# Kernel optimization log

Hardware: AMD Instinct MI355X
Metric: run time of the kernel (lower is better)

Reference implementation:

```python
import jax, jax.numpy as jnp
import numpy as np

BN_EPS = 1e-5

def setup_inputs() -> dict:
    key = jax.random.key(0)
    ks = jax.random.split(key, 4)
    N, C, T, V, H = 32, 64, 512, 25, 3
    x = jax.random.normal(ks[0], (N, C, T, V), dtype=jnp.float32)
    A = jax.random.normal(ks[1], (H, V, V), dtype=jnp.float32)
    # per-head 1x1 conv weights (conv_branch_init-like small std) and biases
    W = jax.random.normal(ks[2], (H, C, C), dtype=jnp.float32) * 0.05
    b = jax.random.normal(ks[3], (H, C), dtype=jnp.float32) * 0.05
    gamma = jnp.ones((C,), dtype=jnp.float32)
    beta = jnp.zeros((C,), dtype=jnp.float32)
    return {"x": x, "A": A, "W": W, "b": b, "gamma": gamma, "beta": beta}

def reference(x, A, W, b, gamma, beta):
    # x: [N,C,T,V], A: [H,V,V], W: [H,Cout,Cin], b: [H,Cout]
    # per-head graph conv: z_h[n,c,t,v] = sum_u A[h,v,u] * x[n,c,t,u]
    z = jnp.einsum('hvu,nctu->hnctv', A, x)
    # per-head 1x1 conv (channel mix) then sum over heads; biases sum too
    out = jnp.einsum('hoc,hnctv->notv', W, z) + b.sum(axis=0)[None, :, None, None]
    # BatchNorm2d (training-mode batch stats, biased variance) over (N,T,V)
    mean = out.mean(axis=(0, 2, 3), keepdims=True)
    var = out.var(axis=(0, 2, 3), keepdims=True)
    out = gamma[None, :, None, None] * (out - mean) * jax.lax.rsqrt(var + BN_EPS) \
          + beta[None, :, None, None]
    # residual (in_channels == out_channels -> identity down) + ReLU
    return jnp.maximum(out + x, 0.0)
```

## Files before the change

kernel.cpp:

```cpp
#include <hip/hip_runtime.h>
#include <hip/hip_bf16.h>

#define N_DIM 32
#define C_DIM 64
#define T_DIM 512
#define V_DIM 25
#define H_DIM 3
#define TT 8
#define GPB 4
#define NBLK1 512
#define NTGRP 2048
#define NTV (N_DIM * T_DIM * V_DIM)
#define NTOT (N_DIM * C_DIM * T_DIM * V_DIM)
#define XPITCH 76
#define XROWS 208
#define TILE_SH 1792
#define SITER 13
#define BN_EPS 1e-5f

typedef float f32x4 __attribute__((ext_vector_type(4)));
typedef short bf16x8 __attribute__((ext_vector_type(8)));
typedef short s16x4 __attribute__((ext_vector_type(4)));

__device__ __forceinline__ short f2bf(float f) {
    __hip_bfloat16 h = __float2bfloat16(f);
    return __builtin_bit_cast(short, h);
}
__device__ __forceinline__ float bf2f(short s) {
    return __uint_as_float(((unsigned)(unsigned short)s) << 16);
}

__device__ __forceinline__ bf16x8 ld_bf8(const short* p) {
    s16x4 a = *(const s16x4*)p;
    s16x4 b = *(const s16x4*)(p + 4);
    bf16x8 r;
    r[0] = a[0]; r[1] = a[1]; r[2] = a[2]; r[3] = a[3];
    r[4] = b[0]; r[5] = b[1]; r[6] = b[2]; r[7] = b[3];
    return r;
}

__global__ __launch_bounds__(256) void gcn_pack(
    const float* __restrict__ A, const float* __restrict__ W,
    short* __restrict__ wpack, short* __restrict__ apack)
{
    const int b   = blockIdx.x;
    const int tid = threadIdx.x;
    const int l15 = tid & 15, hi = (tid >> 4) & 3, w = tid >> 6;
    if (b < 6) {
        int h = b >> 1, s = b & 1;
        const float* wp = W + h * 4096 + (16 * w + l15) * 64 + s * 32 + hi * 8;
        bf16x8 f;
        #pragma unroll
        for (int i = 0; i < 8; ++i) f[i] = f2bf(wp[i]);
        *(bf16x8*)(wpack + ((size_t)b * 256 + tid) * 8) = f;
    } else {
        int bb = b - 6, h = bb >> 1, vt = bb & 1;
        int v = vt * 16 + l15;
        bf16x8 f;
        #pragma unroll
        for (int i = 0; i < 8; ++i) {
            int u = hi * 8 + i;
            f[i] = (v < 25 && u < 25) ? f2bf(A[h * 625 + v * 25 + u]) : (short)0;
        }
        *(bf16x8*)(apack + ((size_t)bb * 256 + tid) * 8) = f;
    }
}

__device__ __forceinline__ void stage_load(float (&fr)[SITER][4],
                                           const float* __restrict__ xg, int tid)
{
    #pragma unroll
    for (int k = 0; k < SITER; ++k) {
        int e = tid + k * 256;
        if (k < SITER - 1 || e < 3200) {
            int cg = e / 200, tu = e - cg * 200;
            const float* p = xg + cg * 51200 + tu;
            fr[k][0] = p[0];
            fr[k][1] = p[12800];
            fr[k][2] = p[25600];
            fr[k][3] = p[38400];
        }
    }
}
__device__ __forceinline__ void stage_write(const float (&fr)[SITER][4],
                                            short* __restrict__ dst, int tid)
{
    #pragma unroll
    for (int k = 0; k < SITER; ++k) {
        int e = tid + k * 256;
        if (k < SITER - 1 || e < 3200) {
            int cg = e / 200, tu = e - cg * 200;
            s16x4 v; v[0] = f2bf(fr[k][0]); v[1] = f2bf(fr[k][1]);
                     v[2] = f2bf(fr[k][2]); v[3] = f2bf(fr[k][3]);
            *(s16x4*)&dst[tu * XPITCH + 4 * cg] = v;
        }
    }
}

template <int SCR>
__global__ __launch_bounds__(256, 2) void gcn_pass1(
    const float* __restrict__ x, const float* __restrict__ A,
    const float* __restrict__ W, const short* __restrict__ wpack,
    const short* __restrict__ apack, void* __restrict__ scratch_,
    float* __restrict__ partial)
{
    __shared__ __align__(16) short x_sT[2][XROWS * XPITCH];

    const int bg   = blockIdx.x;
    const int n    = bg >> 4;
    const int q    = bg & 15;
    const int tid  = threadIdx.x;
    const int lane = tid & 63;
    const int w    = tid >> 6;
    const int l15  = lane & 15;
    const int hi   = lane >> 4;

    bf16x8 wf[H_DIM][2], af[H_DIM][2];
    if constexpr (SCR) {
        #pragma unroll
        for (int h = 0; h < H_DIM; ++h)
            #pragma unroll
            for (int s = 0; s < 2; ++s) {
                wf[h][s] = *(const bf16x8*)(wpack + ((h * 2 + s) * 256 + tid) * 8);
                af[h][s] = *(const bf16x8*)(apack + ((h * 2 + s) * 256 + tid) * 8);
            }
    } else {
        #pragma unroll
        for (int h = 0; h < H_DIM; ++h)
            #pragma unroll
            for (int s = 0; s < 2; ++s) {
                const f32x4* wp = (const f32x4*)(W + h * 4096 + (16 * w + l15) * 64
                                                 + s * 32 + hi * 8);
                f32x4 lo = wp[0], hv = wp[1];
                bf16x8 f;
                #pragma unroll
                for (int i = 0; i < 4; ++i) { f[i] = f2bf(lo[i]); f[4+i] = f2bf(hv[i]); }
                wf[h][s] = f;
                int v = s * 16 + l15;
                bf16x8 g;
                #pragma unroll
                for (int i = 0; i < 8; ++i) {
                    int u = hi * 8 + i;
                    g[i] = (v < 25 && u < 25) ? f2bf(A[h * 625 + v * 25 + u]) : (short)0;
                }
                af[h][s] = g;
            }
    }

    for (int e = tid; e < 304; e += 256) {
        ((int*)&x_sT[0][200 * XPITCH])[e] = 0;
        ((int*)&x_sT[1][200 * XPITCH])[e] = 0;
    }

    const float* xn = x + (size_t)n * 819200;
    float fr[SITER][4];

    stage_load(fr, xn + (q * GPB + 0) * 200, tid);
    stage_write(fr, &x_sT[0][0], tid);
    __syncthreads();

    const int ubase = ((l15 >> 2) * 8) + (l15 & 3);
    const int o_glob = 16 * w + l15;
    float s_tot = 0.f, q_tot = 0.f;

    for (int g = 0; g < GPB; ++g) {
        const int tgrp = q * GPB + g;
        const short* cbuf = &x_sT[g & 1][0];

        if (g < GPB - 1)
            stage_load(fr, xn + (tgrp + 1) * 200, tid);

        #pragma unroll 2
        for (int t = 0; t < TT; ++t) {
            const short* xr0 = &cbuf[(t * 25 + ubase + 0) * XPITCH + hi * 8];
            const short* xr1 = &cbuf[(t * 25 + ubase + 4) * XPITCH + hi * 8];
            const bf16x8 xf00 = ld_bf8(xr0), xf01 = ld_bf8(xr0 + 32);
            const bf16x8 xf10 = ld_bf8(xr1), xf11 = ld_bf8(xr1 + 32);

            f32x4 acc2[2] = {f32x4{0.f,0.f,0.f,0.f}, f32x4{0.f,0.f,0.f,0.f}};

            #pragma unroll
            for (int h = 0; h < H_DIM; ++h) {
                f32x4 y0 = {0.f,0.f,0.f,0.f}, y1 = {0.f,0.f,0.f,0.f};
                y0 = __builtin_amdgcn_mfma_f32_16x16x32_bf16(xf00, wf[h][0], y0, 0,0,0);
                y0 = __builtin_amdgcn_mfma_f32_16x16x32_bf16(xf01, wf[h][1], y0, 0,0,0);
                y1 = __builtin_amdgcn_mfma_f32_16x16x32_bf16(xf10, wf[h][0], y1, 0,0,0);
                y1 = __builtin_amdgcn_mfma_f32_16x16x32_bf16(xf11, wf[h][1], y1, 0,0,0);
                bf16x8 yf;
                #pragma unroll
                for (int j = 0; j < 4; ++j) yf[j] = f2bf(y0[j]);
                #pragma unroll
                for (int j = 0; j < 4; ++j) yf[4 + j] = f2bf(y1[j]);
                acc2[0] = __builtin_amdgcn_mfma_f32_16x16x32_bf16(af[h][0], yf, acc2[0], 0,0,0);
                acc2[1] = __builtin_amdgcn_mfma_f32_16x16x32_bf16(af[h][1], yf, acc2[1], 0,0,0);
            }

            if (SCR) {
                short* base = (short*)scratch_
                            + ((size_t)(n * 512 + tgrp * TT + t)) * TILE_SH;
                s16x4 p0; p0[0]=f2bf(acc2[0][0]); p0[1]=f2bf(acc2[0][1]);
                          p0[2]=f2bf(acc2[0][2]); p0[3]=f2bf(acc2[0][3]);
                *(s16x4*)(base + w * 256 + hi * 64 + l15 * 4) = p0;
                if (hi < 3) {
                    s16x4 p1; p1[0]=f2bf(acc2[1][0]); p1[1]=f2bf(acc2[1][1]);
                              p1[2]=f2bf(acc2[1][2]); p1[3]=f2bf(acc2[1][3]);
                    *(s16x4*)(base + 1024 + w * 192 + hi * 64 + l15 * 4) = p1;
                }
            } else {
                float* op = (float*)scratch_
                          + ((size_t)(n * 64 + o_glob) * 512 + tgrp * TT + t) * 25;
                #pragma unroll
                for (int j = 0; j < 4; ++j) op[hi * 4 + j] = acc2[0][j];
                if (hi < 2) {
                    #pragma unroll
                    for (int j = 0; j < 4; ++j) op[16 + hi * 4 + j] = acc2[1][j];
                } else if (hi == 2) {
                    op[24] = acc2[1][0];
                }
            }

            float s = acc2[0][0] + acc2[0][1] + acc2[0][2] + acc2[0][3];
            float qq = fmaf(acc2[0][0], acc2[0][0], fmaf(acc2[0][1], acc2[0][1],
                       fmaf(acc2[0][2], acc2[0][2], acc2[0][3] * acc2[0][3])));
            if (hi < 2) {
                #pragma unroll
                for (int j = 0; j < 4; ++j) {
                    float v1 = acc2[1][j]; s += v1; qq = fmaf(v1, v1, qq);
                }
            } else if (hi == 2) {
                float v1 = acc2[1][0]; s += v1; qq = fmaf(v1, v1, qq);
            }
            s_tot += s; q_tot += qq;
        }

        if (g < GPB - 1)
            stage_write(fr, &x_sT[(g + 1) & 1][0], tid);
        __syncthreads();
    }

    s_tot += __shfl_xor(s_tot, 16); q_tot += __shfl_xor(q_tot, 16);
    s_tot += __shfl_xor(s_tot, 32); q_tot += __shfl_xor(q_tot, 32);
    if (hi == 0) {
        partial[bg * 128 + o_glob]      = s_tot;
        partial[bg * 128 + 64 + o_glob] = q_tot;
    }
}

__global__ __launch_bounds__(256) void gcn_stats(
    const float* __restrict__ partial, float* __restrict__ stats)
{
    const int o = blockIdx.x;
    const int tid = threadIdx.x;
    float s = 0.f, q = 0.f;
    for (int blk = tid; blk < NBLK1; blk += 256) {
        s += partial[blk * 128 + o];
        q += partial[blk * 128 + 64 + o];
    }
    __shared__ float rs[256], rq[256];
    rs[tid] = s; rq[tid] = q;
    __syncthreads();
    for (int off = 128; off > 0; off >>= 1) {
        if (tid < off) { rs[tid] += rs[tid + off]; rq[tid] += rq[tid + off]; }
        __syncthreads();
    }
    if (tid == 0) {
        float mean = rs[0] / (float)NTV;
        float var  = rq[0] / (float)NTV - mean * mean;
        stats[o]      = mean;
        stats[64 + o] = rsqrtf(var + BN_EPS);
    }
}

__global__ __launch_bounds__(256) void gcn_finalize_b(
    const float* __restrict__ x, const float* __restrict__ gamma,
    const float* __restrict__ beta, const float* __restrict__ stats,
    const short* __restrict__ scr, float* __restrict__ out)
{
    __shared__ __align__(16) short tl_s[8 * TILE_SH];
    const int bid  = blockIdx.x;
    const int n    = bid >> 6;
    const int tgrp = bid & 63;
    const int tid  = threadIdx.x;

    const int4* src = (const int4*)(scr + (size_t)bid * 8 * TILE_SH);
    int4* dst4 = (int4*)tl_s;
    #pragma unroll
    for (int k = 0; k < 7; ++k) dst4[tid + k * 256] = src[tid + k * 256];
    __syncthreads();

    const size_t obase = (size_t)n * 819200 + (size_t)tgrp * 200;
    #pragma unroll
    for (int k = 0; k < 13; ++k) {
        int fi = tid + k * 256;
        if (fi < 3200) {
            int o  = fi / 50;
            int p  = (fi - o * 50) * 4;
            int tl = p / 25;
            int v0 = p - tl * 25;
            float gm = gamma[o] * stats[64 + o];
            float bc = beta[o] - gm * stats[o];
            size_t gidx = obase + (size_t)o * 12800 + p;
            float4 xv = *(const float4*)(x + gidx);
            float r[4];
            #pragma unroll
            for (int j = 0; j < 4; ++j) {
                int vv = v0 + j, tt = tl;
                if (vv >= 25) { vv -= 25; tt += 1; }
                int off = (vv < 16)
                    ? ((o >> 4) * 256 + (vv >> 2) * 64 + (o & 15) * 4 + (vv & 3))
                    : (1024 + (o >> 4) * 192 + ((vv - 16) >> 2) * 64
                       + (o & 15) * 4 + (vv & 3));
                float pv = bf2f(tl_s[tt * TILE_SH + off]);
                r[j] = fmaxf(fmaf(gm, pv, bc) + (&xv.x)[j], 0.f);
            }
            float4 o4; o4.x = r[0]; o4.y = r[1]; o4.z = r[2]; o4.w = r[3];
            *(float4*)(out + gidx) = o4;
        }
    }
}

__global__ __launch_bounds__(256) void gcn_finalize_f(
    const float* __restrict__ x, const float* __restrict__ gamma,
    const float* __restrict__ beta, const float* __restrict__ stats,
    float* __restrict__ out)
{
    const int total4 = NTOT / 4;
    for (int i = blockIdx.x * blockDim.x + threadIdx.x; i < total4;
         i += gridDim.x * blockDim.x) {
        int chan = ((i * 4) / (T_DIM * V_DIM)) & 63;
        float4 p  = ((const float4*)out)[i];
        float4 xv = ((const float4*)x)[i];
        float m = stats[chan], r = stats[64 + chan];
        float g = gamma[chan] * r;
        float bc = beta[chan] - g * m;
        p.x = fmaxf(fmaf(g, p.x, bc) + xv.x, 0.f);
        p.y = fmaxf(fmaf(g, p.y, bc) + xv.y, 0.f);
        p.z = fmaxf(fmaf(g, p.z, bc) + xv.z, 0.f);
        p.w = fmaxf(fmaf(g, p.w, bc) + xv.w, 0.f);
        ((float4*)out)[i] = p;
    }
}

extern "C" void kernel_launch(void* const* d_in, const int* in_sizes, int n_in,
                              void* d_out, int out_size, void* d_ws, size_t ws_size,
                              hipStream_t stream) {
    const float* x     = (const float*)d_in[0];
    const float* A     = (const float*)d_in[1];
    const float* W     = (const float*)d_in[2];
    const float* gamma = (const float*)d_in[4];
    const float* beta  = (const float*)d_in[5];
    float* out = (float*)d_out;

    const size_t scr_bytes   = (size_t)N_DIM * T_DIM * TILE_SH * 2;
    const size_t part_bytes  = (size_t)NBLK1 * 128 * 4;
    const size_t stats_bytes = 512;
    const size_t pack_bytes  = 2 * 6 * 256 * 8 * 2;

    if (ws_size >= scr_bytes + part_bytes + stats_bytes + pack_bytes) {
        short* scr     = (short*)d_ws;
        float* partial = (float*)((char*)d_ws + scr_bytes);
        float* stats   = partial + NBLK1 * 128;
        short* wpack   = (short*)((char*)d_ws + scr_bytes + part_bytes + stats_bytes);
        short* apack   = wpack + 6 * 256 * 8;

        gcn_pack<<<12, 256, 0, stream>>>(A, W, wpack, apack);
        gcn_pass1<1><<<NBLK1, 256, 0, stream>>>(x, A, W, wpack, apack,
                                                (void*)scr, partial);
        gcn_stats<<<64, 256, 0, stream>>>(partial, stats);
        gcn_finalize_b<<<NTGRP, 256, 0, stream>>>(x, gamma, beta, stats, scr, out);
    } else {
        float* partial = (float*)d_ws;
        float* stats   = partial + NBLK1 * 128;
        gcn_pass1<0><<<NBLK1, 256, 0, stream>>>(x, A, W, nullptr, nullptr,
                                                (void*)out, partial);
        gcn_stats<<<64, 256, 0, stream>>>(partial, stats);
        gcn_finalize_f<<<2048, 256, 0, stream>>>(x, gamma, beta, stats, out);
    }
}
```

Measured before the change: 88.41 us.

## Split pass1 into one block per time group and swizzle finalize LDS tile

Pass 1 now launches one block per 8-timestep group (2048 blocks) with a single LDS buffer, instead of 512 blocks that each double-buffer four groups. It also raises the launch-bounds occupancy hint from 2 to 4. This trades away the software pipelining of x loads for more blocks and more resident waves to hide latency. The stats kernel now reduces four times as many partials. The finalize kernel XOR-swizzles 16-byte chunks in shared memory to cut bank conflicts on its scattered bf16 reads.

New measurement: 89.99 us. No clear change (+1.8%).

```diff
diff --git a/kernel.cpp b/kernel.cpp
--- a/kernel.cpp
+++ b/kernel.cpp
@@ -7,8 +7,7 @@
 #define V_DIM 25
 #define H_DIM 3
 #define TT 8
-#define GPB 4
-#define NBLK1 512
+#define NBLK1 2048
 #define NTGRP 2048
 #define NTV (N_DIM * T_DIM * V_DIM)
 #define NTOT (N_DIM * C_DIM * T_DIM * V_DIM)
@@ -98,22 +97,30 @@
 }
 
 template <int SCR>
-__global__ __launch_bounds__(256, 2) void gcn_pass1(
+__global__ __launch_bounds__(256, 4) void gcn_pass1(
     const float* __restrict__ x, const float* __restrict__ A,
     const float* __restrict__ W, const short* __restrict__ wpack,
     const short* __restrict__ apack, void* __restrict__ scratch_,
     float* __restrict__ partial)
 {
-    __shared__ __align__(16) short x_sT[2][XROWS * XPITCH];
-
-    const int bg   = blockIdx.x;
-    const int n    = bg >> 4;
-    const int q    = bg & 15;
+    __shared__ __align__(16) short x_sT[XROWS * XPITCH];
+
+    const int bid  = blockIdx.x;
+    const int n    = bid >> 6;
+    const int tgrp = bid & 63;
     const int tid  = threadIdx.x;
     const int lane = tid & 63;
     const int w    = tid >> 6;
     const int l15  = lane & 15;
     const int hi   = lane >> 4;
+
+    {
+        float fr[SITER][4];
+        stage_load(fr, x + (size_t)n * 819200 + tgrp * (TT * 25), tid);
+        for (int e = tid; e < 304; e += 256)
+            ((int*)&x_sT[200 * XPITCH])[e] = 0;
+        stage_write(fr, &x_sT[0], tid);
+    }
 
     bf16x8 wf[H_DIM][2], af[H_DIM][2];
     if constexpr (SCR) {
@@ -146,103 +153,80 @@
                 af[h][s] = g;
             }
     }
-
-    for (int e = tid; e < 304; e += 256) {
-        ((int*)&x_sT[0][200 * XPITCH])[e] = 0;
-        ((int*)&x_sT[1][200 * XPITCH])[e] = 0;
-    }
-
-    const float* xn = x + (size_t)n * 819200;
-    float fr[SITER][4];
-
-    stage_load(fr, xn + (q * GPB + 0) * 200, tid);
-    stage_write(fr, &x_sT[0][0], tid);
     __syncthreads();
 
     const int ubase = ((l15 >> 2) * 8) + (l15 & 3);
     const int o_glob = 16 * w + l15;
     float s_tot = 0.f, q_tot = 0.f;
 
-    for (int g = 0; g < GPB; ++g) {
-        const int tgrp = q * GPB + g;
-        const short* cbuf = &x_sT[g & 1][0];
-
-        if (g < GPB - 1)
-            stage_load(fr, xn + (tgrp + 1) * 200, tid);
-
-        #pragma unroll 2
-        for (int t = 0; t < TT; ++t) {
-            const short* xr0 = &cbuf[(t * 25 + ubase + 0) * XPITCH + hi * 8];
-            const short* xr1 = &cbuf[(t * 25 + ubase + 4) * XPITCH + hi * 8];
-            const bf16x8 xf00 = ld_bf8(xr0), xf01 = ld_bf8(xr0 + 32);
-            const bf16x8 xf10 = ld_bf8(xr1), xf11 = ld_bf8(xr1 + 32);
-
-            f32x4 acc2[2] = {f32x4{0.f,0.f,0.f,0.f}, f32x4{0.f,0.f,0.f,0.f}};
-
-            #pragma unroll
-            for (int h = 0; h < H_DIM; ++h) {
-                f32x4 y0 = {0.f,0.f,0.f,0.f}, y1 = {0.f,0.f,0.f,0.f};
-                y0 = __builtin_amdgcn_mfma_f32_16x16x32_bf16(xf00, wf[h][0], y0, 0,0,0);
-                y0 = __builtin_amdgcn_mfma_f32_16x16x32_bf16(xf01, wf[h][1], y0, 0,0,0);
-                y1 = __builtin_amdgcn_mfma_f32_16x16x32_bf16(xf10, wf[h][0], y1, 0,0,0);
-                y1 = __builtin_amdgcn_mfma_f32_16x16x32_bf16(xf11, wf[h][1], y1, 0,0,0);
-                bf16x8 yf;
-                #pragma unroll
-                for (int j = 0; j < 4; ++j) yf[j] = f2bf(y0[j]);
-                #pragma unroll
-                for (int j = 0; j < 4; ++j) yf[4 + j] = f2bf(y1[j]);
-                acc2[0] = __builtin_amdgcn_mfma_f32_16x16x32_bf16(af[h][0], yf, acc2[0], 0,0,0);
-                acc2[1] = __builtin_amdgcn_mfma_f32_16x16x32_bf16(af[h][1], yf, acc2[1], 0,0,0);
-            }
-
-            if (SCR) {
-                short* base = (short*)scratch_
-                            + ((size_t)(n * 512 + tgrp * TT + t)) * TILE_SH;
-                s16x4 p0; p0[0]=f2bf(acc2[0][0]); p0[1]=f2bf(acc2[0][1]);
-                          p0[2]=f2bf(acc2[0][2]); p0[3]=f2bf(acc2[0][3]);
-                *(s16x4*)(base + w * 256 + hi * 64 + l15 * 4) = p0;
-                if (hi < 3) {
-                    s16x4 p1; p1[0]=f2bf(acc2[1][0]); p1[1]=f2bf(acc2[1][1]);
-                              p1[2]=f2bf(acc2[1][2]); p1[3]=f2bf(acc2[1][3]);
-                    *(s16x4*)(base + 1024 + w * 192 + hi * 64 + l15 * 4) = p1;
-                }
-            } else {
-                float* op = (float*)scratch_
-                          + ((size_t)(n * 64 + o_glob) * 512 + tgrp * TT + t) * 25;
-                #pragma unroll
-                for (int j = 0; j < 4; ++j) op[hi * 4 + j] = acc2[0][j];
-                if (hi < 2) {
-                    #pragma unroll
-                    for (int j = 0; j < 4; ++j) op[16 + hi * 4 + j] = acc2[1][j];
-                } else if (hi == 2) {
-                    op[24] = acc2[1][0];
-                }
-            }
-
-            float s = acc2[0][0] + acc2[0][1] + acc2[0][2] + acc2[0][3];
-            float qq = fmaf(acc2[0][0], acc2[0][0], fmaf(acc2[0][1], acc2[0][1],
-                       fmaf(acc2[0][2], acc2[0][2], acc2[0][3] * acc2[0][3])));
+    #pragma unroll 2
+    for (int t = 0; t < TT; ++t) {
+        const short* xr0 = &x_sT[(t * 25 + ubase + 0) * XPITCH + hi * 8];
+        const short* xr1 = &x_sT[(t * 25 + ubase + 4) * XPITCH + hi * 8];
+        const bf16x8 xf00 = ld_bf8(xr0), xf01 = ld_bf8(xr0 + 32);
+        const bf16x8 xf10 = ld_bf8(xr1), xf11 = ld_bf8(xr1 + 32);
+
+        f32x4 acc2[2] = {f32x4{0.f,0.f,0.f,0.f}, f32x4{0.f,0.f,0.f,0.f}};
+
+        #pragma unroll
+        for (int h = 0; h < H_DIM; ++h) {
+            f32x4 y0 = {0.f,0.f,0.f,0.f}, y1 = {0.f,0.f,0.f,0.f};
+            y0 = __builtin_amdgcn_mfma_f32_16x16x32_bf16(xf00, wf[h][0], y0, 0,0,0);
+            y0 = __builtin_amdgcn_mfma_f32_16x16x32_bf16(xf01, wf[h][1], y0, 0,0,0);
+            y1 = __builtin_amdgcn_mfma_f32_16x16x32_bf16(xf10, wf[h][0], y1, 0,0,0);
+            y1 = __builtin_amdgcn_mfma_f32_16x16x32_bf16(xf11, wf[h][1], y1, 0,0,0);
+            bf16x8 yf;
+            #pragma unroll
+            for (int j = 0; j < 4; ++j) yf[j] = f2bf(y0[j]);
+            #pragma unroll
+            for (int j = 0; j < 4; ++j) yf[4 + j] = f2bf(y1[j]);
+            acc2[0] = __builtin_amdgcn_mfma_f32_16x16x32_bf16(af[h][0], yf, acc2[0], 0,0,0);
+            acc2[1] = __builtin_amdgcn_mfma_f32_16x16x32_bf16(af[h][1], yf, acc2[1], 0,0,0);
+        }
+
+        if (SCR) {
+            short* base = (short*)scratch_
+                        + ((size_t)(n * 512 + tgrp * TT + t)) * TILE_SH;
+            s16x4 p0; p0[0]=f2bf(acc2[0][0]); p0[1]=f2bf(acc2[0][1]);
+                      p0[2]=f2bf(acc2[0][2]); p0[3]=f2bf(acc2[0][3]);
+            *(s16x4*)(base + w * 256 + hi * 64 + l15 * 4) = p0;
+            if (hi < 3) {
+                s16x4 p1; p1[0]=f2bf(acc2[1][0]); p1[1]=f2bf(acc2[1][1]);
+                          p1[2]=f2bf(acc2[1][2]); p1[3]=f2bf(acc2[1][3]);
+                *(s16x4*)(base + 1024 + w * 192 + hi * 64 + l15 * 4) = p1;
+            }
+        } else {
+            float* op = (float*)scratch_
+                      + ((size_t)(n * 64 + o_glob) * 512 + tgrp * TT + t) * 25;
+            #pragma unroll
+            for (int j = 0; j < 4; ++j) op[hi * 4 + j] = acc2[0][j];
             if (hi < 2) {
                 #pragma unroll
-                for (int j = 0; j < 4; ++j) {
-                    float v1 = acc2[1][j]; s += v1; qq = fmaf(v1, v1, qq);
-                }
+                for (int j = 0; j < 4; ++j) op[16 + hi * 4 + j] = acc2[1][j];
             } else if (hi == 2) {
-                float v1 = acc2[1][0]; s += v1; qq = fmaf(v1, v1, qq);
-            }
-            s_tot += s; q_tot += qq;
-        }
-
-        if (g < GPB - 1)
-            stage_write(fr, &x_sT[(g + 1) & 1][0], tid);
-        __syncthreads();
+                op[24] = acc2[1][0];
+            }
+        }
+
+        float s = acc2[0][0] + acc2[0][1] + acc2[0][2] + acc2[0][3];
+        float qq = fmaf(acc2[0][0], acc2[0][0], fmaf(acc2[0][1], acc2[0][1],
+                   fmaf(acc2[0][2], acc2[0][2], acc2[0][3] * acc2[0][3])));
+        if (hi < 2) {
+            #pragma unroll
+            for (int j = 0; j < 4; ++j) {
+                float v1 = acc2[1][j]; s += v1; qq = fmaf(v1, v1, qq);
+            }
+        } else if (hi == 2) {
+            float v1 = acc2[1][0]; s += v1; qq = fmaf(v1, v1, qq);
+        }
+        s_tot += s; q_tot += qq;
     }
 
     s_tot += __shfl_xor(s_tot, 16); q_tot += __shfl_xor(q_tot, 16);
     s_tot += __shfl_xor(s_tot, 32); q_tot += __shfl_xor(q_tot, 32);
     if (hi == 0) {
-        partial[bg * 128 + o_glob]      = s_tot;
-        partial[bg * 128 + 64 + o_glob] = q_tot;
+        partial[bid * 128 + o_glob]      = s_tot;
+        partial[bid * 128 + 64 + o_glob] = q_tot;
     }
 }
 
@@ -271,6 +255,10 @@
     }
 }
 
+__device__ __forceinline__ int swz16(int chunk) {
+    return chunk ^ ((chunk >> 3) & 7);
+}
+
 __global__ __launch_bounds__(256) void gcn_finalize_b(
     const float* __restrict__ x, const float* __restrict__ gamma,
     const float* __restrict__ beta, const float* __restrict__ stats,
@@ -285,7 +273,10 @@
     const int4* src = (const int4*)(scr + (size_t)bid * 8 * TILE_SH);
     int4* dst4 = (int4*)tl_s;
     #pragma unroll
-    for (int k = 0; k < 7; ++k) dst4[tid + k * 256] = src[tid + k * 256];
+    for (int k = 0; k < 7; ++k) {
+        int i = tid + k * 256;
+        dst4[swz16(i)] = src[i];
+    }
     __syncthreads();
 
     const size_t obase = (size_t)n * 819200 + (size_t)tgrp * 200;
@@ -310,7 +301,9 @@
                     ? ((o >> 4) * 256 + (vv >> 2) * 64 + (o & 15) * 4 + (vv & 3))
                     : (1024 + (o >> 4) * 192 + ((vv - 16) >> 2) * 64
                        + (o & 15) * 4 + (vv & 3));
-                float pv = bf2f(tl_s[tt * TILE_SH + off]);
+                int raw = tt * TILE_SH + off;
+                int adr = swz16(raw >> 3) * 8 + (raw & 7);
+                float pv = bf2f(tl_s[adr]);
                 r[j] = fmaxf(fmaf(gm, pv, bc) + (&xv.x)[j], 0.f);
             }
             float4 o4; o4.x = r[0]; o4.y = r[1]; o4.z = r[2]; o4.w = r[3];
```
